# Optimization experiments

Measured on AMD Instinct MI355X. Metric: run time of the kernel, lower is better.

The kernel has to match this reference:

```python
import jax, jax.numpy as jnp
import numpy as np
from jax import lax

SEQ, BS, D_IN, D_H, D_OUT, N_LAYERS = 784, 256, 1, 512, 1, 3

def _glorot(key, shape):
    fan_in, fan_out = shape[0], shape[1]
    std = jnp.sqrt(2.0 / (fan_in + fan_out))
    return (jax.random.normal(key, shape) * std).astype(jnp.float32)

def setup_inputs() -> dict:
    key = jax.random.key(0)
    ks = jax.random.split(key, 3 + 3 * N_LAYERS + 2)
    x = jax.random.normal(ks[0], (SEQ, BS, D_IN), dtype=jnp.float32)
    W0 = _glorot(ks[1], (D_IN, D_H))
    b0 = jnp.zeros((D_H,), jnp.float32)
    # per-layer recurrence params, stacked: a (L,D_H), B (L,D_H,D_H), C (L,D_H,D_H)
    a = jnp.stack([jax.random.uniform(ks[2 + i], (D_H,), minval=0.999, maxval=1.001) for i in range(N_LAYERS)]).astype(jnp.float32)
    B = jnp.stack([_glorot(ks[2 + N_LAYERS + i], (D_H, D_H)) for i in range(N_LAYERS)])
    C = jnp.stack([_glorot(ks[2 + 2 * N_LAYERS + i], (D_H, D_H)) for i in range(N_LAYERS)])
    Wf = _glorot(ks[2 + 3 * N_LAYERS], (D_H, D_OUT))
    bf = jnp.zeros((D_OUT,), jnp.float32)
    return {"x": x, "W0": W0, "b0": b0, "a": a, "B": B, "C": C, "Wf": Wf, "bf": bf}

def _rnn_layer(x, a_l, B_l, C_l):
    # x: (seq, bs, d_h); diagonal linear recurrence h_t = h_{t-1} * a + x_t @ B
    xb = jnp.einsum('sbi,ih->sbh', x, B_l)  # precompute input projection
    def step(h, xt):
        h = h * a_l + xt
        return h, h
    _, hs = lax.scan(step, jnp.zeros((x.shape[1], a_l.shape[0]), x.dtype), xb)
    return jnp.einsum('sbh,ho->sbo', hs, C_l)

def reference(x, W0, b0, a, B, C, Wf, bf):
    identity = x  # use_downsampling=False, use_residual=True
    h = jax.nn.relu(x @ W0 + b0)
    for l in range(N_LAYERS):
        h = jax.nn.relu(_rnn_layer(h, a[l], B[l], C[l]))
    out = h @ Wf + bf
    return out + identity
```

## Files before the change

kernel.cpp:

```cpp
#include <hip/hip_runtime.h>
#include <hip/hip_bf16.h>

#define SEQ 784
#define BS  256
#define DH  512
#define MT  (SEQ * BS)
#define NL  3
#define NC  14
#define CL  56
#define COLS (BS * DH)

typedef unsigned short u16;
typedef __bf16  bf16x8  __attribute__((ext_vector_type(8)));
typedef float   f32x4   __attribute__((ext_vector_type(4)));
typedef unsigned short u16x8 __attribute__((ext_vector_type(8)));
typedef unsigned short u16x4 __attribute__((ext_vector_type(4)));

__device__ __forceinline__ u16 f2b(float f) {
    unsigned int x = __float_as_uint(f);
    unsigned int r = (x + 0x7FFFu + ((x >> 16) & 1u)) >> 16;
    return (u16)r;
}
__device__ __forceinline__ float b2f(u16 u) {
    return __uint_as_float(((unsigned int)u) << 16);
}

__global__ __launch_bounds__(256) void prep_k(const float* __restrict__ B,
                                              const float* __restrict__ C,
                                              u16* __restrict__ Bp,
                                              u16* __restrict__ Cp)
{
    const long t = (long)blockIdx.x * 256 + threadIdx.x;
    const int  e  = (int)(t & 7);
    const int  l  = (int)((t >> 3) & 63);
    const int  ni = (int)((t >> 9) & 3);
    const int  wd = (int)((t >> 11) & 7);
    const int  g  = (int)((t >> 14) & 15);
    const long lay = t >> 18;
    const int  n = wd * 64 + ni * 16 + (l & 15);
    const int  k = g * 32 + (l >> 4) * 8 + e;
    const long src = (lay << 18) + (long)k * DH + n;
    Bp[t] = f2b(B[src]);
    Cp[t] = f2b(C[src]);
}


#define GEMM_STEP_LOADB(tt)                                                      \
    bf16x8 bv[8];                                                                \
    _Pragma("unroll")                                                            \
    for (int q = 0; q < 8; ++q)                                                  \
        bv[q] = *(const bf16x8*)&Wp[((long)((2 * (tt) + (q >> 2)) * 32 +         \
                                            wid * 4 + (q & 3)) << 9) + (lane << 3)];

#define GEMM_STEP_MFMA(ATILE)                                                    \
    _Pragma("unroll")                                                            \
    for (int kk = 0; kk < 2; ++kk) {                                             \
        const int fcol = ((kk * 4 + (lane >> 4)) ^ (lane & 7)) * 8;              \
        bf16x8 af[4];                                                            \
        _Pragma("unroll")                                                        \
        for (int i = 0; i < 4; ++i)                                              \
            af[i] = *(const bf16x8*)&(ATILE)[(i * 16 + (lane & 15)) * 64 + fcol];\
        _Pragma("unroll")                                                        \
        for (int mi = 0; mi < 4; ++mi)                                           \
            _Pragma("unroll")                                                    \
            for (int ni = 0; ni < 4; ++ni)                                       \
                acc[mi][ni] = __builtin_amdgcn_mfma_f32_16x16x32_bf16(           \
                    af[mi], bv[kk * 4 + ni], acc[mi][ni], 0, 0, 0);              \
    }

template <int RELU>
__global__ __launch_bounds__(512, 4) void gemm_ip(const u16* __restrict__ X,
                                                  const u16* __restrict__ Wp,
                                                  u16* __restrict__ Y)
{
    __shared__ __align__(16) u16 lds[64 * 512];

    const int tid  = threadIdx.x;
    const int lane = tid & 63;
    const int wid  = tid >> 6;
    const long bm  = (long)blockIdx.x * 64;

    const int srow = tid >> 3;
    const int scol = (((tid & 7) ^ (srow & 7)) * 8);
    const u16* gax = X + (bm + srow) * DH + scol;

    f32x4 acc[4][4];
#pragma unroll
    for (int i = 0; i < 4; ++i)
#pragma unroll
        for (int j = 0; j < 4; ++j)
            acc[i][j] = (f32x4){0.f, 0.f, 0.f, 0.f};

    __builtin_amdgcn_global_load_lds(
        (const __attribute__((address_space(1))) void*)gax,
        (__attribute__((address_space(3))) void*)
            ((__attribute__((address_space(3))) char*)lds + tid * 16),
        16, 0, 0);

    for (int t = 0; t < 8; ++t) {
        __syncthreads();
        GEMM_STEP_LOADB(t)
        __builtin_amdgcn_sched_barrier(0);
        if (t < 7) {
            __builtin_amdgcn_global_load_lds(
                (const __attribute__((address_space(1))) void*)(gax + (t + 1) * 64),
                (__attribute__((address_space(3))) void*)
                    ((__attribute__((address_space(3))) char*)lds +
                     ((t + 1) & 1) * 8192 + tid * 16),
                16, 0, 0);
        }
        const u16* Atile = lds + (t & 1) * 4096;
        GEMM_STEP_MFMA(Atile)
    }
    __syncthreads();

    u16* Ctile = lds;
    const int rbase = (lane >> 4) * 4;
    const int cloc  = wid * 64 + (lane & 15);
#pragma unroll
    for (int mi = 0; mi < 4; ++mi)
#pragma unroll
        for (int ni = 0; ni < 4; ++ni)
#pragma unroll
            for (int r = 0; r < 4; ++r) {
                float v = acc[mi][ni][r];
                if (RELU) v = fmaxf(v, 0.f);
                const int row = mi * 16 + rbase + r;
                const int col = (cloc + ni * 16) ^ (((row >> 2) & 3) * 16);
                Ctile[row * 512 + col] = f2b(v);
            }
    __syncthreads();
#pragma unroll
    for (int p = 0; p < 8; ++p) {
        const int e   = p * 4096 + tid * 8;
        const int row = e >> 9;
        const int col = e & 511;
        const int csw = col ^ (((row >> 2) & 3) * 16);
        *(u16x8*)&Y[(bm + row) * DH + col] = *(const u16x8*)&Ctile[row * 512 + csw];
    }
}

__global__ __launch_bounds__(512, 4) void gemm_first(const float* __restrict__ x,
                                                     const float* __restrict__ W0,
                                                     const float* __restrict__ b0,
                                                     const u16* __restrict__ Wp,
                                                     u16* __restrict__ Y)
{
    __shared__ __align__(16) u16 lds[64 * 512];

    const int tid  = threadIdx.x;
    const int lane = tid & 63;
    const int wid  = tid >> 6;
    const long bm  = (long)blockIdx.x * 64;

    const int prow = tid >> 3;
    const int slot = tid & 7;
    const float xv = x[bm + prow];

#pragma unroll
    for (int t = 0; t < 8; ++t) {
        const int k0 = t * 64 + ((slot ^ (prow & 7)) * 8);
        u16x8 o;
#pragma unroll
        for (int e = 0; e < 8; ++e)
            o[e] = f2b(fmaxf(fmaf(xv, W0[k0 + e], b0[k0 + e]), 0.f));
        *(u16x8*)&lds[t * 4096 + tid * 8] = o;
    }

    f32x4 acc[4][4];
#pragma unroll
    for (int i = 0; i < 4; ++i)
#pragma unroll
        for (int j = 0; j < 4; ++j)
            acc[i][j] = (f32x4){0.f, 0.f, 0.f, 0.f};

    __syncthreads();

#pragma unroll
    for (int t = 0; t < 8; ++t) {
        const u16* Atile = lds + t * 4096;
        GEMM_STEP_LOADB(t)
        GEMM_STEP_MFMA(Atile)
    }
    __syncthreads();

    u16* Ctile = lds;
    const int rbase = (lane >> 4) * 4;
    const int cloc  = wid * 64 + (lane & 15);
#pragma unroll
    for (int mi = 0; mi < 4; ++mi)
#pragma unroll
        for (int ni = 0; ni < 4; ++ni)
#pragma unroll
            for (int r = 0; r < 4; ++r) {
                const int row = mi * 16 + rbase + r;
                const int col = (cloc + ni * 16) ^ (((row >> 2) & 3) * 16);
                Ctile[row * 512 + col] = f2b(acc[mi][ni][r]);
            }
    __syncthreads();
#pragma unroll
    for (int p = 0; p < 8; ++p) {
        const int e   = p * 4096 + tid * 8;
        const int row = e >> 9;
        const int col = e & 511;
        const int csw = col ^ (((row >> 2) & 3) * 16);
        *(u16x8*)&Y[(bm + row) * DH + col] = *(const u16x8*)&Ctile[row * 512 + csw];
    }
}

__global__ __launch_bounds__(512, 4) void gemm_last(const u16* __restrict__ X,
                                                    const u16* __restrict__ Wp,
                                                    const float* __restrict__ Wf,
                                                    const float* __restrict__ bf_,
                                                    const float* __restrict__ x,
                                                    float* __restrict__ out)
{
    __shared__ __align__(16) u16 lds[64 * 512];
    float* partials = (float*)lds;

    const int tid  = threadIdx.x;
    const int lane = tid & 63;
    const int wid  = tid >> 6;
    const long bm  = (long)blockIdx.x * 64;

    const int srow = tid >> 3;
    const int scol = (((tid & 7) ^ (srow & 7)) * 8);
    const u16* gax = X + (bm + srow) * DH + scol;

    f32x4 acc[4][4];
#pragma unroll
    for (int i = 0; i < 4; ++i)
#pragma unroll
        for (int j = 0; j < 4; ++j)
            acc[i][j] = (f32x4){0.f, 0.f, 0.f, 0.f};

    __builtin_amdgcn_global_load_lds(
        (const __attribute__((address_space(1))) void*)gax,
        (__attribute__((address_space(3))) void*)
            ((__attribute__((address_space(3))) char*)lds + tid * 16),
        16, 0, 0);

    for (int t = 0; t < 8; ++t) {
        __syncthreads();
        GEMM_STEP_LOADB(t)
        __builtin_amdgcn_sched_barrier(0);
        if (t < 7) {
            __builtin_amdgcn_global_load_lds(
                (const __attribute__((address_space(1))) void*)(gax + (t + 1) * 64),
                (__attribute__((address_space(3))) void*)
                    ((__attribute__((address_space(3))) char*)lds +
                     ((t + 1) & 1) * 8192 + tid * 16),
                16, 0, 0);
        }
        const u16* Atile = lds + (t & 1) * 4096;
        GEMM_STEP_MFMA(Atile)
    }
    __syncthreads();

    const int cbase = wid * 64 + (lane & 15);
    float wf[4];
#pragma unroll
    for (int ni = 0; ni < 4; ++ni) wf[ni] = Wf[cbase + ni * 16];

    float part[4][4];
#pragma unroll
    for (int mi = 0; mi < 4; ++mi)
#pragma unroll
        for (int r = 0; r < 4; ++r) {
            float s = 0.f;
#pragma unroll
            for (int ni = 0; ni < 4; ++ni)
                s = fmaf(fmaxf(acc[mi][ni][r], 0.f), wf[ni], s);
            part[mi][r] = s;
        }
#pragma unroll
    for (int mi = 0; mi < 4; ++mi)
#pragma unroll
        for (int r = 0; r < 4; ++r) {
#pragma unroll
            for (int off = 1; off < 16; off <<= 1)
                part[mi][r] += __shfl_xor(part[mi][r], off, 64);
        }
    if ((lane & 15) == 0) {
        const int q = lane >> 4;
#pragma unroll
        for (int mi = 0; mi < 4; ++mi)
#pragma unroll
            for (int r = 0; r < 4; ++r)
                partials[wid * 64 + mi * 16 + q * 4 + r] = part[mi][r];
    }
    __syncthreads();
    if (tid < 64) {
        float s = 0.f;
#pragma unroll
        for (int w = 0; w < 8; ++w) s += partials[w * 64 + tid];
        out[bm + tid] = s + bf_[0] + x[bm + tid];
    }
}

__global__ __launch_bounds__(256) void scanA_k(const u16* __restrict__ buf,
                                               const float* __restrict__ a_all,
                                               int layer,
                                               float* __restrict__ carry)
{
    const long T   = (long)blockIdx.x * 256 + threadIdx.x;
    const int col4 = (int)(T & (COLS / 4 - 1)) * 4;
    const int c    = (int)(T >> 15);
    const f32x4 av = *(const f32x4*)&a_all[layer * DH + (col4 & (DH - 1))];
    const u16* p = buf + (long)c * CL * COLS + col4;

    float h[4] = {0.f, 0.f, 0.f, 0.f};
    u16x4 pre[8];
#pragma unroll
    for (int i = 0; i < 8; ++i) pre[i] = *(const u16x4*)&p[(long)i * COLS];
    for (int s8 = 0; s8 < CL; s8 += 8) {
        const bool more = (s8 + 8) < CL;
#pragma unroll
        for (int j = 0; j < 8; ++j) {
            const u16x4 v = pre[j];
            if (more) pre[j] = *(const u16x4*)&p[(long)(s8 + 8 + j) * COLS];
#pragma unroll
            for (int i = 0; i < 4; ++i)
                h[i] = fmaf(h[i], av[i], b2f((u16)v[i]));
        }
    }
    *(f32x4*)&carry[(long)c * COLS + col4] = (f32x4){h[0], h[1], h[2], h[3]};
}

__global__ __launch_bounds__(256) void scanB_k(float* __restrict__ carry,
                                               const float* __restrict__ a_all,
                                               int layer)
{
    const int col = blockIdx.x * 256 + threadIdx.x;
    const float av = a_all[layer * DH + (col & (DH - 1))];
    float a2 = av * av, a4 = a2 * a2, a8 = a4 * a4;
    float a16 = a8 * a8, a32 = a16 * a16;
    const float pw = a32 * a16 * a8;

    float cin = 0.f;
    for (int c = 0; c < NC; ++c) {
        float cr = carry[(long)c * COLS + col];
        carry[(long)c * COLS + col] = cin;
        cin = fmaf(cin, pw, cr);
    }
}

__global__ __launch_bounds__(256) void scanC_k(u16* __restrict__ buf,
                                               const float* __restrict__ a_all,
                                               int layer,
                                               const float* __restrict__ carry)
{
    const long T   = (long)blockIdx.x * 256 + threadIdx.x;
    const int col4 = (int)(T & (COLS / 4 - 1)) * 4;
    const int c    = (int)(T >> 15);
    const f32x4 av = *(const f32x4*)&a_all[layer * DH + (col4 & (DH - 1))];
    u16* p = buf + (long)c * CL * COLS + col4;

    const f32x4 ci = *(const f32x4*)&carry[(long)c * COLS + col4];
    float h[4] = {ci[0], ci[1], ci[2], ci[3]};
    u16x4 pre[8];
#pragma unroll
    for (int i = 0; i < 8; ++i) pre[i] = *(const u16x4*)&p[(long)i * COLS];
    for (int s8 = 0; s8 < CL; s8 += 8) {
        const bool more = (s8 + 8) < CL;
#pragma unroll
        for (int j = 0; j < 8; ++j) {
            const u16x4 v = pre[j];
            if (more) pre[j] = *(const u16x4*)&p[(long)(s8 + 8 + j) * COLS];
            u16x4 o;
#pragma unroll
            for (int i = 0; i < 4; ++i) {
                h[i] = fmaf(h[i], av[i], b2f((u16)v[i]));
                o[i] = f2b(h[i]);
            }
            *(u16x4*)&p[(long)(s8 + j) * COLS] = o;
        }
    }
}

extern "C" void kernel_launch(void* const* d_in, const int* in_sizes, int n_in,
                              void* d_out, int out_size, void* d_ws, size_t ws_size,
                              hipStream_t stream)
{
    const float* x   = (const float*)d_in[0];
    const float* W0  = (const float*)d_in[1];
    const float* b0  = (const float*)d_in[2];
    const float* a   = (const float*)d_in[3];
    const float* B   = (const float*)d_in[4];
    const float* C   = (const float*)d_in[5];
    const float* Wf  = (const float*)d_in[6];
    const float* bf_ = (const float*)d_in[7];
    float* out = (float*)d_out;

    const long BUF = (long)MT * DH;
    const size_t need = (size_t)BUF * 2 + 2ULL * 3 * DH * DH * 2
                      + (size_t)NC * COLS * 4;
    if (ws_size < need) return;

    u16*   buf   = (u16*)d_ws;
    u16*   Bp    = buf + BUF;
    u16*   Cp    = Bp + 3L * DH * DH;
    float* carry = (float*)(Cp + 3L * DH * DH);

    prep_k<<<(3 * DH * DH) / 256, 256, 0, stream>>>(B, C, Bp, Cp);

    for (int l = 0; l < NL; ++l) {
        if (l == 0)
            gemm_first<<<MT / 64, 512, 0, stream>>>(x, W0, b0, Bp, buf);
        else
            gemm_ip<0><<<MT / 64, 512, 0, stream>>>(buf, Bp + (long)l * DH * DH, buf);

        scanA_k<<<(NC * COLS / 4) / 256, 256, 0, stream>>>(buf, a, l, carry);
        scanB_k<<<COLS / 256, 256, 0, stream>>>(carry, a, l);
        scanC_k<<<(NC * COLS / 4) / 256, 256, 0, stream>>>(buf, a, l, carry);

        if (l == NL - 1)
            gemm_last<<<MT / 64, 512, 0, stream>>>(buf, Cp + (long)l * DH * DH,
                                                   Wf, bf_, x, out);
        else
            gemm_ip<1><<<MT / 64, 512, 0, stream>>>(buf, Cp + (long)l * DH * DH, buf);
    }
}
```

Before: 957.7 us.

## Fuse carry scan into scanC and load B fragments per k-substep

Removes the scanB kernel launch: each scanC thread now recomputes its incoming chunk carry by serially folding all previous chunk carries with a^56. This adds redundant global reads of up to 13 carries per thread but saves one launch and a dependent pass. Separately, the GEMM kernels now load B weight fragments per kk substep (4 vectors instead of 8) and drop the sched_barrier, which lowers register pressure but may expose load latency.

```diff
diff --git a/kernel.cpp b/kernel.cpp
--- a/kernel.cpp
+++ b/kernel.cpp
@@ -45,16 +45,15 @@
 }
 
 
-#define GEMM_STEP_LOADB(tt)                                                      \
-    bf16x8 bv[8];                                                                \
-    _Pragma("unroll")                                                            \
-    for (int q = 0; q < 8; ++q)                                                  \
-        bv[q] = *(const bf16x8*)&Wp[((long)((2 * (tt) + (q >> 2)) * 32 +         \
-                                            wid * 4 + (q & 3)) << 9) + (lane << 3)];
-
-#define GEMM_STEP_MFMA(ATILE)                                                    \
+#define GEMM_STEP_KK(ATILE, tt)                                                  \
     _Pragma("unroll")                                                            \
     for (int kk = 0; kk < 2; ++kk) {                                             \
+        bf16x8 bv[4];                                                            \
+        _Pragma("unroll")                                                        \
+        for (int ni = 0; ni < 4; ++ni)                                           \
+            bv[ni] = *(const bf16x8*)&Wp[((long)((2 * (tt) + kk) * 32 +          \
+                                                 wid * 4 + ni) << 9) +           \
+                                         (lane << 3)];                           \
         const int fcol = ((kk * 4 + (lane >> 4)) ^ (lane & 7)) * 8;              \
         bf16x8 af[4];                                                            \
         _Pragma("unroll")                                                        \
@@ -65,7 +64,7 @@
             _Pragma("unroll")                                                    \
             for (int ni = 0; ni < 4; ++ni)                                       \
                 acc[mi][ni] = __builtin_amdgcn_mfma_f32_16x16x32_bf16(           \
-                    af[mi], bv[kk * 4 + ni], acc[mi][ni], 0, 0, 0);              \
+                    af[mi], bv[ni], acc[mi][ni], 0, 0, 0);                       \
     }
 
 template <int RELU>
@@ -99,8 +98,6 @@
 
     for (int t = 0; t < 8; ++t) {
         __syncthreads();
-        GEMM_STEP_LOADB(t)
-        __builtin_amdgcn_sched_barrier(0);
         if (t < 7) {
             __builtin_amdgcn_global_load_lds(
                 (const __attribute__((address_space(1))) void*)(gax + (t + 1) * 64),
@@ -110,7 +107,7 @@
                 16, 0, 0);
         }
         const u16* Atile = lds + (t & 1) * 4096;
-        GEMM_STEP_MFMA(Atile)
+        GEMM_STEP_KK(Atile, t)
     }
     __syncthreads();
 
@@ -179,8 +176,7 @@
 #pragma unroll
     for (int t = 0; t < 8; ++t) {
         const u16* Atile = lds + t * 4096;
-        GEMM_STEP_LOADB(t)
-        GEMM_STEP_MFMA(Atile)
+        GEMM_STEP_KK(Atile, t)
     }
     __syncthreads();
 
@@ -242,8 +238,6 @@
 
     for (int t = 0; t < 8; ++t) {
         __syncthreads();
-        GEMM_STEP_LOADB(t)
-        __builtin_amdgcn_sched_barrier(0);
         if (t < 7) {
             __builtin_amdgcn_global_load_lds(
                 (const __attribute__((address_space(1))) void*)(gax + (t + 1) * 64),
@@ -253,7 +247,7 @@
                 16, 0, 0);
         }
         const u16* Atile = lds + (t & 1) * 4096;
-        GEMM_STEP_MFMA(Atile)
+        GEMM_STEP_KK(Atile, t)
     }
     __syncthreads();
 
@@ -327,24 +321,6 @@
     *(f32x4*)&carry[(long)c * COLS + col4] = (f32x4){h[0], h[1], h[2], h[3]};
 }
 
-__global__ __launch_bounds__(256) void scanB_k(float* __restrict__ carry,
-                                               const float* __restrict__ a_all,
-                                               int layer)
-{
-    const int col = blockIdx.x * 256 + threadIdx.x;
-    const float av = a_all[layer * DH + (col & (DH - 1))];
-    float a2 = av * av, a4 = a2 * a2, a8 = a4 * a4;
-    float a16 = a8 * a8, a32 = a16 * a16;
-    const float pw = a32 * a16 * a8;
-
-    float cin = 0.f;
-    for (int c = 0; c < NC; ++c) {
-        float cr = carry[(long)c * COLS + col];
-        carry[(long)c * COLS + col] = cin;
-        cin = fmaf(cin, pw, cr);
-    }
-}
-
 __global__ __launch_bounds__(256) void scanC_k(u16* __restrict__ buf,
                                                const float* __restrict__ a_all,
                                                int layer,
@@ -356,8 +332,25 @@
     const f32x4 av = *(const f32x4*)&a_all[layer * DH + (col4 & (DH - 1))];
     u16* p = buf + (long)c * CL * COLS + col4;
 
-    const f32x4 ci = *(const f32x4*)&carry[(long)c * COLS + col4];
-    float h[4] = {ci[0], ci[1], ci[2], ci[3]};
+    float h[4];
+#pragma unroll
+    for (int i = 0; i < 4; ++i) h[i] = 0.f;
+    {
+        float pw[4];
+#pragma unroll
+        for (int i = 0; i < 4; ++i) {
+            float a2 = av[i] * av[i], a4 = a2 * a2, a8 = a4 * a4;
+            float a16 = a8 * a8, a32 = a16 * a16;
+            pw[i] = a32 * a16 * a8;
+        }
+        for (int cc = 0; cc < c; ++cc) {
+            const f32x4 cr = *(const f32x4*)&carry[(long)cc * COLS + col4];
+#pragma unroll
+            for (int i = 0; i < 4; ++i)
+                h[i] = fmaf(h[i], pw[i], cr[i]);
+        }
+    }
+
     u16x4 pre[8];
 #pragma unroll
     for (int i = 0; i < 8; ++i) pre[i] = *(const u16x4*)&p[(long)i * COLS];
@@ -411,7 +404,6 @@
             gemm_ip<0><<<MT / 64, 512, 0, stream>>>(buf, Bp + (long)l * DH * DH, buf);
 
         scanA_k<<<(NC * COLS / 4) / 256, 256, 0, stream>>>(buf, a, l, carry);
-        scanB_k<<<COLS / 256, 256, 0, stream>>>(carry, a, l);
         scanC_k<<<(NC * COLS / 4) / 256, 256, 0, stream>>>(buf, a, l, carry);
 
         if (l == NL - 1)
```

After: 928.9 us. 1.03x faster.
